# Kernel tuning notes

Measured on AMD Instinct MI355X. Metric: run time of the kernel, lower is better.

## Reference

```python
import jax, jax.numpy as jnp
import numpy as np

C = 64
CQ = C // 8


def setup_inputs() -> dict:
    key = jax.random.key(0)
    ks = jax.random.split(key, 8)
    x = jax.random.normal(ks[0], (8, C, 64, 64), dtype=jnp.float32)
    s = 1.0 / np.sqrt(C)
    Wq = jax.random.normal(ks[1], (CQ, C), dtype=jnp.float32) * s
    bq = jax.random.normal(ks[2], (CQ,), dtype=jnp.float32) * s
    Wk = jax.random.normal(ks[3], (CQ, C), dtype=jnp.float32) * s
    bk = jax.random.normal(ks[4], (CQ,), dtype=jnp.float32) * s
    Wv = jax.random.normal(ks[5], (C, C), dtype=jnp.float32) * s
    bv = jax.random.normal(ks[6], (C,), dtype=jnp.float32) * s
    gamma = jnp.array([0.5], dtype=jnp.float32)  # nonzero so value path contributes
    return {"x": x, "Wq": Wq, "bq": bq, "Wk": Wk, "bk": bk, "Wv": Wv, "bv": bv, "gamma": gamma}


def reference(x, Wq, bq, Wk, bk, Wv, bv, gamma):
    B, Cc, H, W = x.shape
    xf = x.reshape(B, Cc, H * W)  # [B, C, N]
    # 1x1 conv == channel-mixing linear
    f = jnp.einsum('oc,bcn->bon', Wq, xf) + bq[None, :, None]  # [B, C/8, N]
    g = jnp.einsum('oc,bcn->bon', Wk, xf) + bk[None, :, None]  # [B, C/8, N]
    h = jnp.einsum('oc,bcn->bon', Wv, xf) + bv[None, :, None]  # [B, C, N]
    # scores[b,i,j] = f[b,:,i] . g[b,:,j]; softmax over dim=1 (query dim i)
    scores = jnp.einsum('bdi,bdj->bij', f, g)  # [B, N, N]
    beta = jax.nn.softmax(scores, axis=1)
    o = gamma[0] * jnp.einsum('bcn,bnm->bcm', h, beta) + xf
    return o.reshape(B, Cc, H, W)
```

## Files before the change

### kernel.cpp

```cpp
#include <hip/hip_runtime.h>
#include <hip/hip_fp16.h>


typedef _Float16 half8_t __attribute__((ext_vector_type(8)));
typedef _Float16 half4_t __attribute__((ext_vector_type(4)));
typedef _Float16 half2_t __attribute__((ext_vector_type(2)));
typedef __fp16  fp16x2  __attribute__((ext_vector_type(2)));
typedef float float4_t __attribute__((ext_vector_type(4)));
typedef unsigned int uintx4 __attribute__((ext_vector_type(4)));

#define NTOK 4096
#define PRH 72
#define LOG2E 1.44269504088896340736f

#if __has_builtin(__builtin_amdgcn_exp2f)
__device__ __forceinline__ float fexp2(float x) { return __builtin_amdgcn_exp2f(x); }
#else
__device__ __forceinline__ float fexp2(float x) { return exp2f(x); }
#endif

__device__ __forceinline__ half2_t pkcvt(float a, float b) {
    fp16x2 v = __builtin_amdgcn_cvt_pkrtz(a, b);
    return __builtin_bit_cast(half2_t, v);
}

__device__ __forceinline__ float4_t mfma16(half4_t a, half4_t b, float4_t c) {
    return __builtin_amdgcn_mfma_f32_16x16x16f16(a, b, c, 0, 0, 0);
}
__device__ __forceinline__ float4_t mfma32(half8_t a, half8_t b, float4_t c) {
    return __builtin_amdgcn_mfma_f32_16x16x32_f16(a, b, c, 0, 0, 0);
}

#define GLDS(G, L) __builtin_amdgcn_global_load_lds(                            \
    (const __attribute__((address_space(1))) unsigned int*)(G),                 \
    (__attribute__((address_space(3))) unsigned int*)(L), 16, 0, 0)

#define WAITVM4_BAR() do {                                                      \
    __builtin_amdgcn_sched_barrier(0);                                          \
    asm volatile("s_waitcnt vmcnt(4)" ::: "memory");                            \
    __builtin_amdgcn_sched_barrier(0);                                          \
    __builtin_amdgcn_s_barrier();                                               \
} while (0)

__global__ __launch_bounds__(320) void proj_kernel(
    const float* __restrict__ x,
    const float* __restrict__ Wq, const float* __restrict__ bq,
    const float* __restrict__ Wk, const float* __restrict__ bk,
    const float* __restrict__ Wv, const float* __restrict__ bv,
    __half* __restrict__ fTR, __half* __restrict__ gT16, __half* __restrict__ hM)
{
    __shared__ __align__(16) _Float16 xh[32 * PRH];
    const int t      = threadIdx.x;
    const int blk    = blockIdx.x;
    const int b      = blockIdx.y;
    const int n0     = blk * 32;
    const int kt64   = blk >> 1;
    const int t4base = (blk & 1) * 2;

    if (t < 256) {
#pragma unroll
        for (int i = 0; i < 2; i++) {
            const int idx = t + i * 256;
            const int c = idx >> 3, f4 = idx & 7;
            float4 v = *(const float4*)(x + (((size_t)(b * 64 + c)) << 12) + n0 + f4 * 4);
            const int cs = c ^ ((f4 & 3) << 4);
            xh[(f4 * 4 + 0) * PRH + cs] = (_Float16)v.x;
            xh[(f4 * 4 + 1) * PRH + cs] = (_Float16)v.y;
            xh[(f4 * 4 + 2) * PRH + cs] = (_Float16)v.z;
            xh[(f4 * 4 + 3) * PRH + cs] = (_Float16)v.w;
        }
    }

    const int w    = t >> 6;
    const int lane = t & 63;
    const int q    = lane >> 4;
    const int ml   = lane & 15;

    const float* wrow;
    if (w == 0) wrow = (ml < 8) ? (Wq + ml * 64) : (Wk + (ml - 8) * 64);
    else        wrow = Wv + ((w - 1) * 16 + ml) * 64;
    half4_t afr[4];
#pragma unroll
    for (int ks = 0; ks < 4; ks++) {
        float4 wv4 = *(const float4*)(wrow + ks * 16 + q * 4);
        afr[ks] = (half4_t){(_Float16)wv4.x, (_Float16)wv4.y,
                            (_Float16)wv4.z, (_Float16)wv4.w};
    }
    float4 bias4;
    if (w == 0) bias4 = (q < 2) ? *(const float4*)(bq + q * 4)
                                : *(const float4*)(bk + (q - 2) * 4);
    else        bias4 = *(const float4*)(bv + (w - 1) * 16 + q * 4);

    __syncthreads();

    float4_t acc2[2];
#pragma unroll
    for (int cg = 0; cg < 2; cg++) {
        const int tok  = cg * 16 + ml;
        const int swz  = (tok >> 2) & 3;
        float4_t acc = (float4_t){0.f, 0.f, 0.f, 0.f};
#pragma unroll
        for (int ks = 0; ks < 4; ks++) {
            half4_t bfr = *(const half4_t*)(&xh[tok * PRH + ((ks ^ swz) * 16 + q * 4)]);
            acc = __builtin_amdgcn_mfma_f32_16x16x16f16(afr[ks], bfr, acc, 0, 0, 0);
        }
        acc[0] += bias4.x; acc[1] += bias4.y; acc[2] += bias4.z; acc[3] += bias4.w;
        acc2[cg] = acc;
        const int gtok = n0 + tok;
        const int t4   = t4base + cg;

        if (w == 0) {
            __half* rec = fTR + ((size_t)b << 16) + (size_t)(kt64 * 16 + ml) * 64;
            if (q < 2) {
                half4_t fv = {(_Float16)(acc[0] * LOG2E), (_Float16)(acc[1] * LOG2E),
                              (_Float16)(acc[2] * LOG2E), (_Float16)(acc[3] * LOG2E)};
                *(half4_t*)(rec + q * 16 + t4 * 4) = fv;
            } else {
                half4_t cv = (half4_t){};
                if (q == 2) cv[0] = (_Float16)1.0f;
                *(half4_t*)(rec + q * 16 + t4 * 4) = cv;
            }
            float gn2p = acc[0] * acc[0] + acc[1] * acc[1] +
                         acc[2] * acc[2] + acc[3] * acc[3];
            float gn2 = gn2p + __shfl_xor(gn2p, 16, 64);
            if (q >= 2) {
                half4_t gv = {(_Float16)acc[0], (_Float16)acc[1],
                              (_Float16)acc[2], (_Float16)acc[3]};
                __half* gp = gT16 + (size_t)((b << 12) + gtok) * 16;
                *(half4_t*)(gp + (q - 2) * 4) = gv;
                if (q == 2) {
                    const float M = (LOG2E * 4.6f) * __builtin_sqrtf(gn2) + 1.0f;
                    *(half4_t*)(gp + 8) = (half4_t){(_Float16)(-M), 0, 0, 0};
                } else {
                    *(half4_t*)(gp + 12) = (half4_t){};
                }
            }
        }
    }

    __syncthreads();
    if (w > 0) {
        const int ch = (w - 1) * 16 + q * 4;
#pragma unroll
        for (int cg = 0; cg < 2; cg++) {
            const int loc = ((ml >> 2) << 3) + (cg << 2) + (ml & 3);
#pragma unroll
            for (int r = 0; r < 4; r++)
                xh[(ch + r) * 36 + loc] = (_Float16)acc2[cg][r];
        }
    }
    __syncthreads();
    if (t < 256) {
        const int ch   = t >> 2;
        const int part = t & 3;
        half8_t v = *(const half8_t*)(&xh[ch * 36 + part * 8]);
        __half* dst = hM + ((size_t)(b * 64 + ch) << 12) + (size_t)kt64 * 64
                         + (blk & 1) * 32 + part * 8;
        *(half8_t*)dst = v;
    }
}


#define LDAH(V0, V1, V2, V3, HP)                                                \
    half8_t V0 = *(const half8_t*)(HP);                                         \
    half8_t V1 = *(const half8_t*)((HP) + 1024);                                \
    half8_t V2 = *(const half8_t*)((HP) + 2048);                                \
    half8_t V3 = *(const half8_t*)((HP) + 3072);

#define QK(F, N)                                                                \
    float4_t N##A0, N##B0, N##A1, N##B1;                                        \
    {                                                                           \
        half4_t a0 = __builtin_shufflevector(F, F, 0, 1, 2, 3);                 \
        half4_t a1 = __builtin_shufflevector(F, F, 4, 5, 6, 7);                 \
        __builtin_amdgcn_s_setprio(1);                                          \
        N##A0 = mfma16(a0, gfA, z4);                                            \
        N##B0 = mfma16(a0, gfB, z4);                                            \
        N##A1 = mfma16(a1, gfA, z4);                                            \
        N##B1 = mfma16(a1, gfB, z4);                                            \
        __builtin_amdgcn_s_setprio(0);                                          \
    }

#define PAIRC(N, H0, H1, H2, H3)                                                \
    {                                                                           \
        float eA0 = fexp2(N##A0[0]), eA1 = fexp2(N##A0[1]),                     \
              eA2 = fexp2(N##A0[2]), eA3 = fexp2(N##A0[3]);                     \
        float oA0 = fexp2(N##A1[0]), oA1 = fexp2(N##A1[1]),                     \
              oA2 = fexp2(N##A1[2]), oA3 = fexp2(N##A1[3]);                     \
        float eB0 = fexp2(N##B0[0]), eB1 = fexp2(N##B0[1]),                     \
              eB2 = fexp2(N##B0[2]), eB3 = fexp2(N##B0[3]);                     \
        float oB0 = fexp2(N##B1[0]), oB1 = fexp2(N##B1[1]),                     \
              oB2 = fexp2(N##B1[2]), oB3 = fexp2(N##B1[3]);                     \
        uintx4 puA = {__builtin_bit_cast(unsigned int, pkcvt(eA0, eA1)),        \
                      __builtin_bit_cast(unsigned int, pkcvt(eA2, eA3)),        \
                      __builtin_bit_cast(unsigned int, pkcvt(oA0, oA1)),        \
                      __builtin_bit_cast(unsigned int, pkcvt(oA2, oA3))};       \
        uintx4 puB = {__builtin_bit_cast(unsigned int, pkcvt(eB0, eB1)),        \
                      __builtin_bit_cast(unsigned int, pkcvt(eB2, eB3)),        \
                      __builtin_bit_cast(unsigned int, pkcvt(oB0, oB1)),        \
                      __builtin_bit_cast(unsigned int, pkcvt(oB2, oB3))};       \
        half8_t pA8 = __builtin_bit_cast(half8_t, puA);                         \
        half8_t pB8 = __builtin_bit_cast(half8_t, puB);                         \
        __builtin_amdgcn_s_setprio(1);                                          \
        accLA = mfma32(ones8, pA8, accLA);                                      \
        accLB = mfma32(ones8, pB8, accLB);                                      \
        accA[0] = mfma32(H0, pA8, accA[0]); accB[0] = mfma32(H0, pB8, accB[0]); \
        accA[1] = mfma32(H1, pA8, accA[1]); accB[1] = mfma32(H1, pB8, accB[1]); \
        accA[2] = mfma32(H2, pA8, accA[2]); accB[2] = mfma32(H2, pB8, accB[2]); \
        accA[3] = mfma32(H3, pA8, accA[3]); accB[3] = mfma32(H3, pB8, accB[3]); \
        __builtin_amdgcn_s_setprio(0);                                          \
    }

template<int NT>
__global__ __launch_bounds__(256) void attn_kernel(
    const __half* __restrict__ fTR, const __half* __restrict__ gT16,
    const __half* __restrict__ hM,
    __half* __restrict__ Pacc, float* __restrict__ Lsum)
{
    __shared__ __align__(16) _Float16 hl[2][8192];
    const int tid   = threadIdx.x;
    const int w     = tid >> 6;
    const int lane  = tid & 63;
    const int q     = lane >> 4;
    const int ml    = lane & 15;
    const int m7    = ml & 7;
    const int b     = blockIdx.y;
    const int split = blockIdx.z;
    const int colA  = blockIdx.x * 128 + w * 16 + ml;
    const int colB  = colA + 64;

    half4_t gfA = *(const half4_t*)(gT16 + ((size_t)((b << 12) + colA)) * 16 + q * 4);
    half4_t gfB = *(const half4_t*)(gT16 + ((size_t)((b << 12) + colB)) * 16 + q * 4);

    float4_t accA[4], accB[4];
#pragma unroll
    for (int cg = 0; cg < 4; cg++) {
        accA[cg] = (float4_t){0.f, 0.f, 0.f, 0.f};
        accB[cg] = (float4_t){0.f, 0.f, 0.f, 0.f};
    }
    float4_t accLA = (float4_t){0.f, 0.f, 0.f, 0.f};
    float4_t accLB = (float4_t){0.f, 0.f, 0.f, 0.f};
    const half8_t ones8 = {(_Float16)1.0f, (_Float16)1.0f, (_Float16)1.0f,
                           (_Float16)1.0f, (_Float16)1.0f, (_Float16)1.0f,
                           (_Float16)1.0f, (_Float16)1.0f};
    const float4_t z4 = (float4_t){0.f, 0.f, 0.f, 0.f};

    const int k64 = split * NT * 2;

    const int ch0  = tid >> 3;
    const int gsw  = (tid & 7) ^ (ch0 & 7);
    const __half* hs0 = hM + ((size_t)(b * 64 + ch0) << 12) + (size_t)k64 * 64 + gsw * 8;
    const __half* hs1 = hs0 + ((size_t)32 << 12);
    const __half* fptr = fTR + ((size_t)b << 16) + (size_t)(k64 * 16 + ml) * 64 + q * 16;

    const int gxa = ((q ^ m7) << 3);
    const int gxb = (((4 + q) ^ m7) << 3);

    GLDS(hs0,      &hl[0][tid * 8]);
    GLDS(hs1,      &hl[0][2048 + tid * 8]);
    GLDS(hs0 + 64, &hl[0][4096 + tid * 8]);
    GLDS(hs1 + 64, &hl[0][6144 + tid * 8]);
    half8_t f01 = *(const half8_t*)fptr;
    half8_t f23 = *(const half8_t*)(fptr + 8);
    half8_t f45 = *(const half8_t*)(fptr + 1024);
    half8_t f67 = *(const half8_t*)(fptr + 1032);
    __syncthreads();

    const __half* hn0 = hs0 + 128;
    const __half* hn1 = hs1 + 128;

#pragma unroll 1
    for (int kt = 0; kt < NT; kt++) {
        const _Float16* hbA = &hl[kt & 1][ml << 6];
        const _Float16* hbB = hbA + 4096;

        LDAH(a00, a01, a02, a03, hbA + gxa)
        QK(f01, s)

        if (kt + 1 < NT) {
            _Float16* nb = &hl[(kt + 1) & 1][0];
            GLDS(hn0,      nb + tid * 8);
            GLDS(hn1,      nb + 2048 + tid * 8);
            GLDS(hn0 + 64, nb + 4096 + tid * 8);
            GLDS(hn1 + 64, nb + 6144 + tid * 8);
            hn0 += 128;
            hn1 += 128;
        }

        LDAH(a10, a11, a12, a13, hbA + gxb)
        QK(f23, t)

        PAIRC(s, a00, a01, a02, a03)

        LDAH(a20, a21, a22, a23, hbB + gxa)

        PAIRC(t, a10, a11, a12, a13)

        QK(f45, u)
        LDAH(a30, a31, a32, a33, hbB + gxb)

        PAIRC(u, a20, a21, a22, a23)

        QK(f67, v)
        if (kt + 1 < NT) {
            f01 = *(const half8_t*)(fptr + 2048);
            f23 = *(const half8_t*)(fptr + 2056);
            f45 = *(const half8_t*)(fptr + 3072);
            f67 = *(const half8_t*)(fptr + 3080);
            fptr += 2048;
        }

        PAIRC(v, a30, a31, a32, a33)

        if (kt + 1 < NT) {
            WAITVM4_BAR();
        }
    }

    __half* pa = Pacc + (((size_t)(split * 8 + b) * 64) << 12);
#pragma unroll
    for (int cg = 0; cg < 4; cg++)
#pragma unroll
        for (int r = 0; r < 4; r++) {
            int ch = cg * 16 + q * 4 + r;
            pa[((size_t)ch << 12) + colA] = __float2half(accA[cg][r]);
            pa[((size_t)ch << 12) + colB] = __float2half(accB[cg][r]);
        }
    if (q == 0) {
        Lsum[((size_t)(split * 8 + b) << 12) + colA] = accLA[0];
        Lsum[((size_t)(split * 8 + b) << 12) + colB] = accLB[0];
    }
}

template<int S>
__global__ __launch_bounds__(256) void merge_kernel(
    const __half* __restrict__ Pacc, const float* __restrict__ Lsum,
    const float* __restrict__ x, const float* __restrict__ gammap,
    float* __restrict__ out)
{
    __shared__ float invL[64];
    const int tid  = threadIdx.x;
    const int c4   = tid & 15;
    const int chh  = tid >> 4;
    const int b    = blockIdx.y;
    const int col0 = blockIdx.x * 64;
    const int ch   = blockIdx.z * 16 + chh;

    if (tid < 64) {
        float L = 0.f;
#pragma unroll
        for (int s = 0; s < S; s++)
            L += Lsum[((size_t)(s * 8 + b) << 12) + col0 + tid];
        invL[tid] = gammap[0] / L;
    }
    __syncthreads();

    const int cc = c4 * 4;
    const size_t base = (((size_t)b * 64 + ch) << 12) + col0 + cc;
    float4 xv = *(const float4*)(x + base);
    float o0 = 0.f, o1 = 0.f, o2 = 0.f, o3 = 0.f;
#pragma unroll
    for (int s = 0; s < S; s++) {
        half4_t pv = *(const half4_t*)(Pacc +
            (((size_t)(s * 8 + b) * 64 + ch) << 12) + col0 + cc);
        o0 += (float)pv[0];
        o1 += (float)pv[1];
        o2 += (float)pv[2];
        o3 += (float)pv[3];
    }
    float4 ov;
    ov.x = o0 * invL[cc]     + xv.x;
    ov.y = o1 * invL[cc + 1] + xv.y;
    ov.z = o2 * invL[cc + 2] + xv.z;
    ov.w = o3 * invL[cc + 3] + xv.w;
    *(float4*)(out + base) = ov;
}

extern "C" void kernel_launch(void* const* d_in, const int* in_sizes, int n_in,
                              void* d_out, int out_size, void* d_ws, size_t ws_size,
                              hipStream_t stream) {
    const float* x     = (const float*)d_in[0];
    const float* Wq    = (const float*)d_in[1];
    const float* bq    = (const float*)d_in[2];
    const float* Wk    = (const float*)d_in[3];
    const float* bk    = (const float*)d_in[4];
    const float* Wv    = (const float*)d_in[5];
    const float* bv    = (const float*)d_in[6];
    const float* gamma = (const float*)d_in[7];
    float* out = (float*)d_out;

    const size_t fr_bytes  = (size_t)8 * 65536 * 2;
    const size_t g_bytes   = (size_t)8 * NTOK * 16 * 2;
    const size_t hM_bytes  = (size_t)8 * 64 * NTOK * 2;
    const size_t pa_split  = (size_t)8 * 64 * NTOK * 2;
    const size_t l_split   = (size_t)8 * NTOK * sizeof(float);
    const size_t base_need = fr_bytes + g_bytes + hM_bytes;

    int S = 1;
    if (ws_size >= base_need + 4 * (pa_split + l_split)) S = 4;
    else if (ws_size >= base_need + 2 * (pa_split + l_split)) S = 2;

    char* p = (char*)d_ws;
    __half* fTR  = (__half*)p;  p += fr_bytes;
    __half* gT16 = (__half*)p;  p += g_bytes;
    __half* hM   = (__half*)p;  p += hM_bytes;
    __half* Pacc = (__half*)p;  p += (size_t)S * pa_split;
    float*  Lsum = (float*)p;

    proj_kernel<<<dim3(128, 8), 320, 0, stream>>>(x, Wq, bq, Wk, bk, Wv, bv,
                                                  fTR, gT16, hM);
    if (S == 4) {
        attn_kernel<8><<<dim3(32, 8, 4), 256, 0, stream>>>(fTR, gT16, hM, Pacc, Lsum);
        merge_kernel<4><<<dim3(64, 8, 4), 256, 0, stream>>>(Pacc, Lsum, x, gamma, out);
    } else if (S == 2) {
        attn_kernel<16><<<dim3(32, 8, 2), 256, 0, stream>>>(fTR, gT16, hM, Pacc, Lsum);
        merge_kernel<2><<<dim3(64, 8, 4), 256, 0, stream>>>(Pacc, Lsum, x, gamma, out);
    } else {
        attn_kernel<32><<<dim3(32, 8, 1), 256, 0, stream>>>(fTR, gT16, hM, Pacc, Lsum);
        merge_kernel<1><<<dim3(64, 8, 4), 256, 0, stream>>>(Pacc, Lsum, x, gamma, out);
    }
}
```

Baseline: 114.5 us.

## Cut attention register pressure, compute row sums with VALU, remap block order

The softmax denominator was computed with extra MFMAs against a ones vector. It is now accumulated with scalar adds, and lanes are reduced with shuffles at the end. The LDS loads of H fragments are interleaved just before each use so fewer are live at once, f45/f67 are loaded per iteration, and launch bounds request 4 blocks per CU. Blocks are also remapped so consecutive launches share the same column block across batches and splits. Lowering register pressure should raise occupancy and remove MFMA work, at the cost of more VALU adds and less prefetch slack, since vmcnt is tightened to 2.

```diff
diff --git a/kernel.cpp b/kernel.cpp
--- a/kernel.cpp
+++ b/kernel.cpp
@@ -35,9 +35,9 @@
     (const __attribute__((address_space(1))) unsigned int*)(G),                 \
     (__attribute__((address_space(3))) unsigned int*)(L), 16, 0, 0)
 
-#define WAITVM4_BAR() do {                                                      \
+#define WAITVM2_BAR() do {                                                      \
     __builtin_amdgcn_sched_barrier(0);                                          \
-    asm volatile("s_waitcnt vmcnt(4)" ::: "memory");                            \
+    asm volatile("s_waitcnt vmcnt(2)" ::: "memory");                            \
     __builtin_amdgcn_sched_barrier(0);                                          \
     __builtin_amdgcn_s_barrier();                                               \
 } while (0)
@@ -190,6 +190,8 @@
               eB2 = fexp2(N##B0[2]), eB3 = fexp2(N##B0[3]);                     \
         float oB0 = fexp2(N##B1[0]), oB1 = fexp2(N##B1[1]),                     \
               oB2 = fexp2(N##B1[2]), oB3 = fexp2(N##B1[3]);                     \
+        lpA += ((eA0 + eA1) + (eA2 + eA3)) + ((oA0 + oA1) + (oA2 + oA3));       \
+        lpB += ((eB0 + eB1) + (eB2 + eB3)) + ((oB0 + oB1) + (oB2 + oB3));       \
         uintx4 puA = {__builtin_bit_cast(unsigned int, pkcvt(eA0, eA1)),        \
                       __builtin_bit_cast(unsigned int, pkcvt(eA2, eA3)),        \
                       __builtin_bit_cast(unsigned int, pkcvt(oA0, oA1)),        \
@@ -201,8 +203,6 @@
         half8_t pA8 = __builtin_bit_cast(half8_t, puA);                         \
         half8_t pB8 = __builtin_bit_cast(half8_t, puB);                         \
         __builtin_amdgcn_s_setprio(1);                                          \
-        accLA = mfma32(ones8, pA8, accLA);                                      \
-        accLB = mfma32(ones8, pB8, accLB);                                      \
         accA[0] = mfma32(H0, pA8, accA[0]); accB[0] = mfma32(H0, pB8, accB[0]); \
         accA[1] = mfma32(H1, pA8, accA[1]); accB[1] = mfma32(H1, pB8, accB[1]); \
         accA[2] = mfma32(H2, pA8, accA[2]); accB[2] = mfma32(H2, pB8, accB[2]); \
@@ -210,8 +210,8 @@
         __builtin_amdgcn_s_setprio(0);                                          \
     }
 
-template<int NT>
-__global__ __launch_bounds__(256) void attn_kernel(
+template<int NT, int S>
+__global__ __launch_bounds__(256, 4) void attn_kernel(
     const __half* __restrict__ fTR, const __half* __restrict__ gT16,
     const __half* __restrict__ hM,
     __half* __restrict__ Pacc, float* __restrict__ Lsum)
@@ -223,9 +223,15 @@
     const int q     = lane >> 4;
     const int ml    = lane & 15;
     const int m7    = ml & 7;
-    const int b     = blockIdx.y;
-    const int split = blockIdx.z;
-    const int colA  = blockIdx.x * 128 + w * 16 + ml;
+
+    const int lin   = blockIdx.x + ((int)blockIdx.y << 5) + ((int)blockIdx.z << 8);
+    constexpr int NG = 8 * S;
+    const int grp   = lin & (NG - 1);
+    const int cb    = lin / NG;
+    const int b     = grp / S;
+    const int split = grp % S;
+
+    const int colA  = cb * 128 + w * 16 + ml;
     const int colB  = colA + 64;
 
     half4_t gfA = *(const half4_t*)(gT16 + ((size_t)((b << 12) + colA)) * 16 + q * 4);
@@ -237,11 +243,7 @@
         accA[cg] = (float4_t){0.f, 0.f, 0.f, 0.f};
         accB[cg] = (float4_t){0.f, 0.f, 0.f, 0.f};
     }
-    float4_t accLA = (float4_t){0.f, 0.f, 0.f, 0.f};
-    float4_t accLB = (float4_t){0.f, 0.f, 0.f, 0.f};
-    const half8_t ones8 = {(_Float16)1.0f, (_Float16)1.0f, (_Float16)1.0f,
-                           (_Float16)1.0f, (_Float16)1.0f, (_Float16)1.0f,
-                           (_Float16)1.0f, (_Float16)1.0f};
+    float lpA = 0.f, lpB = 0.f;
     const float4_t z4 = (float4_t){0.f, 0.f, 0.f, 0.f};
 
     const int k64 = split * NT * 2;
@@ -261,8 +263,6 @@
     GLDS(hs1 + 64, &hl[0][6144 + tid * 8]);
     half8_t f01 = *(const half8_t*)fptr;
     half8_t f23 = *(const half8_t*)(fptr + 8);
-    half8_t f45 = *(const half8_t*)(fptr + 1024);
-    half8_t f67 = *(const half8_t*)(fptr + 1032);
     __syncthreads();
 
     const __half* hn0 = hs0 + 128;
@@ -273,9 +273,10 @@
         const _Float16* hbA = &hl[kt & 1][ml << 6];
         const _Float16* hbB = hbA + 4096;
 
-        LDAH(a00, a01, a02, a03, hbA + gxa)
         QK(f01, s)
 
+        half8_t f45 = *(const half8_t*)(fptr + 1024);
+        half8_t f67 = *(const half8_t*)(fptr + 1032);
         if (kt + 1 < NT) {
             _Float16* nb = &hl[(kt + 1) & 1][0];
             GLDS(hn0,      nb + tid * 8);
@@ -286,35 +287,37 @@
             hn1 += 128;
         }
 
-        LDAH(a10, a11, a12, a13, hbA + gxb)
+        LDAH(a0, a1, a2, a3, hbA + gxa)
+        PAIRC(s, a0, a1, a2, a3)
+
         QK(f23, t)
-
-        PAIRC(s, a00, a01, a02, a03)
-
-        LDAH(a20, a21, a22, a23, hbB + gxa)
-
-        PAIRC(t, a10, a11, a12, a13)
+        LDAH(b0, b1, b2, b3, hbA + gxb)
+        PAIRC(t, b0, b1, b2, b3)
 
         QK(f45, u)
-        LDAH(a30, a31, a32, a33, hbB + gxb)
-
-        PAIRC(u, a20, a21, a22, a23)
+        LDAH(c0, c1, c2, c3, hbB + gxa)
+        PAIRC(u, c0, c1, c2, c3)
 
         QK(f67, v)
+        LDAH(d0, d1, d2, d3, hbB + gxb)
         if (kt + 1 < NT) {
             f01 = *(const half8_t*)(fptr + 2048);
             f23 = *(const half8_t*)(fptr + 2056);
-            f45 = *(const half8_t*)(fptr + 3072);
-            f67 = *(const half8_t*)(fptr + 3080);
             fptr += 2048;
         }
-
-        PAIRC(v, a30, a31, a32, a33)
+        PAIRC(v, d0, d1, d2, d3)
 
         if (kt + 1 < NT) {
-            WAITVM4_BAR();
-        }
-    }
+            WAITVM2_BAR();
+        }
+    }
+
+    float lA = lpA;
+    lA += __shfl_xor(lA, 16, 64);
+    lA += __shfl_xor(lA, 32, 64);
+    float lB = lpB;
+    lB += __shfl_xor(lB, 16, 64);
+    lB += __shfl_xor(lB, 32, 64);
 
     __half* pa = Pacc + (((size_t)(split * 8 + b) * 64) << 12);
 #pragma unroll
@@ -326,8 +329,8 @@
             pa[((size_t)ch << 12) + colB] = __float2half(accB[cg][r]);
         }
     if (q == 0) {
-        Lsum[((size_t)(split * 8 + b) << 12) + colA] = accLA[0];
-        Lsum[((size_t)(split * 8 + b) << 12) + colB] = accLB[0];
+        Lsum[((size_t)(split * 8 + b) << 12) + colA] = lA;
+        Lsum[((size_t)(split * 8 + b) << 12) + colB] = lB;
     }
 }
 
@@ -409,13 +412,13 @@
     proj_kernel<<<dim3(128, 8), 320, 0, stream>>>(x, Wq, bq, Wk, bk, Wv, bv,
                                                   fTR, gT16, hM);
     if (S == 4) {
-        attn_kernel<8><<<dim3(32, 8, 4), 256, 0, stream>>>(fTR, gT16, hM, Pacc, Lsum);
+        attn_kernel<8, 4><<<dim3(32, 8, 4), 256, 0, stream>>>(fTR, gT16, hM, Pacc, Lsum);
         merge_kernel<4><<<dim3(64, 8, 4), 256, 0, stream>>>(Pacc, Lsum, x, gamma, out);
     } else if (S == 2) {
-        attn_kernel<16><<<dim3(32, 8, 2), 256, 0, stream>>>(fTR, gT16, hM, Pacc, Lsum);
+        attn_kernel<16, 2><<<dim3(32, 8, 2), 256, 0, stream>>>(fTR, gT16, hM, Pacc, Lsum);
         merge_kernel<2><<<dim3(64, 8, 4), 256, 0, stream>>>(Pacc, Lsum, x, gamma, out);
     } else {
-        attn_kernel<32><<<dim3(32, 8, 1), 256, 0, stream>>>(fTR, gT16, hM, Pacc, Lsum);
+        attn_kernel<32, 1><<<dim3(32, 8, 1), 256, 0, stream>>>(fTR, gT16, hM, Pacc, Lsum);
         merge_kernel<1><<<dim3(64, 8, 4), 256, 0, stream>>>(Pacc, Lsum, x, gamma, out);
     }
 }
```

New measurement: 154.6 us. +35.0%, slower.
